# Performance work log

Measured on AMD Instinct MI355X. Metric: run time of the kernel, lower is better.

The kernel has to match this reference:

```python
import jax, jax.numpy as jnp
import numpy as np

EMB_SIZE = 768
BLOCK_SIZE = 64
OFFSET = 1  # bert cls offset


def setup_inputs() -> dict:
    key = jax.random.key(0)
    ks = jax.random.split(key, 10)
    n, c, d, h, E, M, P = 4, 1024, 768, 12, 42, 8, 1024
    sequence_output = jax.random.normal(ks[0], (n, c, d), jnp.float32)
    attention = jax.random.uniform(ks[1], (n, h, c, c), jnp.float32)
    attention = attention / attention.sum(-1, keepdims=True)  # softmax-like rows
    Wh = jax.random.normal(ks[2], (EMB_SIZE, 2 * d), jnp.float32) * 0.02
    bh = jax.random.normal(ks[3], (EMB_SIZE,), jnp.float32) * 0.02
    Wt = jax.random.normal(ks[4], (EMB_SIZE, 2 * d), jnp.float32) * 0.02
    bt = jax.random.normal(ks[5], (EMB_SIZE,), jnp.float32) * 0.02
    Wb = jax.random.normal(ks[6], (99, EMB_SIZE * BLOCK_SIZE), jnp.float32) * 0.02
    mention_pos = jax.random.randint(ks[7], (n, E, M), 0, c - 1 - OFFSET, jnp.int32)
    mention_mask = jax.random.randint(ks[8], (n, E, M), 0, 2, jnp.int32)
    mention_mask = mention_mask.at[:, :, 0].set(1)  # every entity has >=1 mention
    hts = jax.random.randint(ks[9], (n, P, 2), 0, E, jnp.int32)
    return {"sequence_output": sequence_output, "attention": attention,
            "Wh": Wh, "bh": bh, "Wt": Wt, "bt": bt, "Wb": Wb,
            "mention_pos": mention_pos, "mention_mask": mention_mask, "hts": hts}


def _get_hrt_doc(seq, att, pos, mask, ht):
    # seq [c,d], att [h,c,c], pos/mask [E,M], ht [P,2]
    p = pos + OFFSET                                   # [E,M]
    valid = mask > 0
    memb = seq[p]                                      # [E,M,d] gather
    e_emb = jax.scipy.special.logsumexp(
        jnp.where(valid[..., None], memb, -jnp.inf), axis=1)  # [E,d]
    matt = att[:, p]                                   # [h,E,M,c] gather
    cnt = valid.sum(1).astype(seq.dtype)               # [E]
    e_att = (matt * valid[None, :, :, None].astype(seq.dtype)).sum(2)
    e_att = jnp.transpose(e_att, (1, 0, 2)) / cnt[:, None, None]  # [E,h,c] mention mean
    hs = e_emb[ht[:, 0]]                               # [P,d]
    ts = e_emb[ht[:, 1]]
    h_att = e_att[ht[:, 0]]                            # [P,h,c]
    t_att = e_att[ht[:, 1]]
    ht_att = (h_att * t_att).mean(1)                   # [P,c] head mean
    ht_att = ht_att / (ht_att.sum(1, keepdims=True) + 1e-5)
    rs = jnp.einsum('ld,rl->rd', seq, ht_att)          # [P,d]
    return hs, ts, rs


def reference(sequence_output, attention, Wh, bh, Wt, bt, Wb,
              mention_pos, mention_mask, hts):
    d = sequence_output.shape[-1]
    hs, ts, rs = jax.vmap(_get_hrt_doc)(sequence_output, attention,
                                        mention_pos, mention_mask, hts)
    hs = hs.reshape(-1, d)
    ts = ts.reshape(-1, d)
    rs = rs.reshape(-1, d)
    hs = jnp.tanh(jnp.concatenate([hs, rs], axis=1) @ Wh.T + bh)
    ts = jnp.tanh(jnp.concatenate([ts, rs], axis=1) @ Wt.T + bt)
    nb = EMB_SIZE // BLOCK_SIZE
    b1 = hs.reshape(-1, nb, BLOCK_SIZE)
    b2 = ts.reshape(-1, nb, BLOCK_SIZE)
    bl = (b1[:, :, :, None] * b2[:, :, None, :]).reshape(-1, EMB_SIZE * BLOCK_SIZE)
    logits = bl @ Wb.T                                 # [N, num_labels+2]
    return logits
```

## Files before the change

kernel.cpp:

```cpp
#include <hip/hip_runtime.h>
#include <hip/hip_bf16.h>
#include <hip/hip_fp16.h>
#include <math.h>

#define NDOC 4
#define CCC  1024
#define DDD  768
#define HHH  12
#define EEE  42
#define MMM  8
#define PPP  1024
#define NK   99
#define NPAD 112
#define NSLICE 24

typedef __attribute__((ext_vector_type(8))) short short8v;
typedef __attribute__((ext_vector_type(8))) _Float16 half8;
typedef __attribute__((ext_vector_type(4))) float floatx4;

__device__ __forceinline__ unsigned short f32_to_bf16u(float f) {
  return __builtin_bit_cast(unsigned short, __float2bfloat16(f));
}
__device__ __forceinline__ unsigned short f32_to_f16u(float f) {
  return __builtin_bit_cast(unsigned short, __float2half(f));
}

__global__ __launch_bounds__(256) void k_prep(
    const float* __restrict__ seq, const float* __restrict__ att,
    const float* __restrict__ Wh, const float* __restrict__ Wt,
    const float* __restrict__ Wb,
    const int* __restrict__ pos, const int* __restrict__ mask,
    unsigned short* __restrict__ eembB, float* __restrict__ eatt,
    unsigned short* __restrict__ WhtB, unsigned short* __restrict__ seqTB,
    unsigned short* __restrict__ WpB) {
  const int bx = blockIdx.x;
  const int tid = threadIdx.x;
  if (bx < 168) {
    int e = bx % EEE, doc = bx / EEE;
    int base = (doc*EEE + e)*MMM;
    int p[MMM], mk[MMM];
#pragma unroll
    for (int m = 0; m < MMM; ++m) { p[m] = pos[base+m] + 1; mk[m] = mask[base+m]; }
    for (int d0 = tid; d0 < DDD; d0 += 256) {
      float v[MMM]; float mx = -INFINITY;
#pragma unroll
      for (int m = 0; m < MMM; ++m) {
        v[m] = seq[(doc*CCC + p[m])*DDD + d0];
        if (mk[m]) mx = fmaxf(mx, v[m]);
      }
      float s = 0.f;
#pragma unroll
      for (int m = 0; m < MMM; ++m) if (mk[m]) s += expf(v[m]-mx);
      eembB[(doc*EEE + e)*DDD + d0] = f32_to_bf16u(logf(s) + mx);
    }
  } else if (bx < 2184) {
    int b = bx - 168;
    int head = b % HHH, e = (b/HHH) % EEE, doc = b / (HHH*EEE);
    int base = (doc*EEE + e)*MMM;
    int j = tid * 4;
    float ax=0.f, ay=0.f, az=0.f, aw=0.f; float cnt = 0.f;
#pragma unroll
    for (int m = 0; m < MMM; ++m) {
      int mk = mask[base+m];
      cnt += (float)mk;
      if (mk) {
        int pp = pos[base+m] + 1;
        const float4 a = *(const float4*)&att[((size_t)(doc*HHH + head)*CCC + pp)*CCC + j];
        ax += a.x; ay += a.y; az += a.z; aw += a.w;
      }
    }
    float inv = 1.f / cnt;
    float4 o; o.x = ax*inv; o.y = ay*inv; o.z = az*inv; o.w = aw*inv;
    *(float4*)&eatt[((size_t)((doc*EEE + e)*HHH + head))*CCC + j] = o;
  } else if (bx < 3336) {
    int gid = (bx - 2184)*256 + tid;
    int half = gid >= 147456;
    int loc = half ? gid - 147456 : gid;
    const float* src = (half ? Wt : Wh) + (size_t)loc*8;
    float4 v0 = *(const float4*)src;
    float4 v1 = *(const float4*)(src+4);
    unsigned short o[8];
    o[0]=f32_to_bf16u(v0.x); o[1]=f32_to_bf16u(v0.y); o[2]=f32_to_bf16u(v0.z); o[3]=f32_to_bf16u(v0.w);
    o[4]=f32_to_bf16u(v1.x); o[5]=f32_to_bf16u(v1.y); o[6]=f32_to_bf16u(v1.z); o[7]=f32_to_bf16u(v1.w);
    *(uint4*)&WhtB[(size_t)half*1179648 + (size_t)loc*8] = *(const uint4*)o;
  } else if (bx < 4104) {
    __shared__ float tl[64][65];
    int b = bx - 3336;
    int d0 = (b % 12)*64, c0 = ((b/12) % 16)*64, doc = b / 192;
#pragma unroll
    for (int rep = 0; rep < 4; ++rep) {
      int cr = rep*16 + (tid >> 4);
      int d4 = (tid & 15) * 4;
      float4 v = *(const float4*)&seq[((size_t)doc*CCC + c0 + cr)*DDD + d0 + d4];
      tl[cr][d4+0]=v.x; tl[cr][d4+1]=v.y; tl[cr][d4+2]=v.z; tl[cr][d4+3]=v.w;
    }
    __syncthreads();
#pragma unroll
    for (int rep = 0; rep < 4; ++rep) {
      int dr = rep*16 + (tid >> 4);
      int c4 = (tid & 15) * 4;
      unsigned short o[4];
#pragma unroll
      for (int kq = 0; kq < 4; ++kq)
        o[kq] = f32_to_bf16u(tl[c4+kq][dr]);
      *(uint2*)&seqTB[((size_t)doc*DDD + d0 + dr)*CCC + c0 + c4] = *(const uint2*)o;
    }
  } else {
    int t = (bx - 4104)*256 + tid;
    int j8 = (t & 7) * 8;
    int n = (t >> 3) % NPAD;
    int ki = t / 896;
    unsigned short o[8];
    if (n < NK) {
      const float* src = &Wb[(size_t)n*49152 + ki*64 + j8];
      float4 v0 = *(const float4*)src;
      float4 v1 = *(const float4*)(src+4);
      o[0]=f32_to_f16u(v0.x); o[1]=f32_to_f16u(v0.y); o[2]=f32_to_f16u(v0.z); o[3]=f32_to_f16u(v0.w);
      o[4]=f32_to_f16u(v1.x); o[5]=f32_to_f16u(v1.y); o[6]=f32_to_f16u(v1.z); o[7]=f32_to_f16u(v1.w);
    } else {
#pragma unroll
      for (int e=0;e<8;++e) o[e]=0;
    }
    int js = (t & 7) >> 2, q = t & 3;
    int nt = n >> 4, lnn = n & 15;
    int c = ((js*7 + nt)*4 + q)*16 + lnn;
    *(uint4*)&WpB[(size_t)ki*7168 + c*8] = *(const uint4*)o;
  }
}

__global__ __launch_bounds__(256) void k_htatt1(const float* __restrict__ eatt,
    const int* __restrict__ hts, float* __restrict__ htU,
    float* __restrict__ Ssum) {
  __shared__ float tile[EEE*16*12];
  const int cg = blockIdx.x, doc = blockIdx.y;
  const int c0 = cg * 16;
  for (int idx = threadIdx.x; idx < EEE*16*12; idx += 256) {
    int e = idx / 192, rem = idx % 192, h = rem / 16, cc = rem % 16;
    tile[(e*16 + cc)*12 + h] =
        eatt[((size_t)((doc*EEE + e)*HHH + h))*CCC + c0 + cc];
  }
  __syncthreads();
  const int cc = threadIdx.x & 15;
  const int pg = threadIdx.x >> 4;
  for (int it = 0; it < 64; ++it) {
    int p = pg + it*16;
    int h0 = hts[(doc*PPP + p)*2 + 0];
    int t0 = hts[(doc*PPP + p)*2 + 1];
    const float* a = &tile[(h0*16 + cc)*12];
    const float* b = &tile[(t0*16 + cc)*12];
    float4 a0 = *(const float4*)a,     b0 = *(const float4*)b;
    float4 a1 = *(const float4*)(a+4), b1 = *(const float4*)(b+4);
    float4 a2 = *(const float4*)(a+8), b2 = *(const float4*)(b+8);
    float s = a0.x*b0.x + a0.y*b0.y + a0.z*b0.z + a0.w*b0.w
            + a1.x*b1.x + a1.y*b1.y + a1.z*b1.z + a1.w*b1.w
            + a2.x*b2.x + a2.y*b2.y + a2.z*b2.z + a2.w*b2.w;
    s *= (1.f/12.f);
    htU[((size_t)(doc*PPP + p))*CCC + c0 + cc] = s;
    float r = s;
    r += __shfl_xor(r, 1, 16);
    r += __shfl_xor(r, 2, 16);
    r += __shfl_xor(r, 4, 16);
    r += __shfl_xor(r, 8, 16);
    if (cc == 0) Ssum[((size_t)(doc*PPP + p))*64 + cg] = r;
  }
}

__global__ __launch_bounds__(256) void k_htnorm(const float* __restrict__ htU,
    const float* __restrict__ Ssum, unsigned short* __restrict__ htB) {
  __shared__ float sc_sh;
  const int b = blockIdx.x;
  const int lane = threadIdx.x;
  if (lane < 64) {
    float r = Ssum[(size_t)b*64 + lane];
    for (int off = 32; off > 0; off >>= 1) r += __shfl_down(r, off, 64);
    if (lane == 0) sc_sh = 1.f / (r + 1e-5f);
  }
  __syncthreads();
  float sc = sc_sh;
  float4 v = *(const float4*)&htU[(size_t)b*CCC + lane*4];
  unsigned short o[4];
  o[0] = f32_to_bf16u(v.x*sc); o[1] = f32_to_bf16u(v.y*sc);
  o[2] = f32_to_bf16u(v.z*sc); o[3] = f32_to_bf16u(v.w*sc);
  *(uint2*)&htB[(size_t)b*CCC + lane*4] = *(const uint2*)o;
}

__global__ __launch_bounds__(256) void k_rs_mfma(
    const unsigned short* __restrict__ htB,
    const unsigned short* __restrict__ seqTB,
    unsigned short* __restrict__ rsB) {
  __shared__ unsigned short A_l[4096];
  __shared__ unsigned short B_l[4096];
  const int n0 = blockIdx.x * 128;
  const int m0 = blockIdx.y * 128;
  const int doc = m0 >> 10;
  const int mloc = m0 & 1023;
  const int t = threadIdx.x;
  const int lane = t & 63;
  const int ln = lane & 15, q4 = lane >> 4;
  const int w = t >> 6;
  const int wr = w >> 1, wc = w & 1;

  const int r0 = t >> 2;
  const int koff = (t & 3) * 8;
  const unsigned short* srcA0 = htB + ((size_t)doc*CCC + mloc + r0)*CCC + koff;
  const unsigned short* srcA1 = htB + ((size_t)doc*CCC + mloc + r0 + 64)*CCC + koff;
  const unsigned short* srcB0 = seqTB + ((size_t)doc*DDD + n0 + r0)*CCC + koff;
  const unsigned short* srcB1 = seqTB + ((size_t)doc*DDD + n0 + r0 + 64)*CCC + koff;

  floatx4 acc[4][4];
#pragma unroll
  for (int i = 0; i < 4; ++i)
#pragma unroll
    for (int j = 0; j < 4; ++j) acc[i][j] = (floatx4){0.f,0.f,0.f,0.f};

  for (int k0 = 0; k0 < CCC; k0 += 32) {
    uint4 va0 = *(const uint4*)(srcA0 + k0);
    uint4 va1 = *(const uint4*)(srcA1 + k0);
    uint4 vb0 = *(const uint4*)(srcB0 + k0);
    uint4 vb1 = *(const uint4*)(srcB1 + k0);
    __syncthreads();
    *(uint4*)&A_l[(size_t)t*8]       = va0;
    *(uint4*)&A_l[(size_t)(t+256)*8] = va1;
    *(uint4*)&B_l[(size_t)t*8]       = vb0;
    *(uint4*)&B_l[(size_t)(t+256)*8] = vb1;
    __syncthreads();
    short8v a[4], b[4];
#pragma unroll
    for (int rt = 0; rt < 4; ++rt)
      a[rt] = *(const short8v*)&A_l[((wr*64 + rt*16 + ln)*4 + q4)*8];
#pragma unroll
    for (int nt = 0; nt < 4; ++nt)
      b[nt] = *(const short8v*)&B_l[((wc*64 + nt*16 + ln)*4 + q4)*8];
#pragma unroll
    for (int rt = 0; rt < 4; ++rt)
#pragma unroll
      for (int nt = 0; nt < 4; ++nt)
        acc[rt][nt] = __builtin_amdgcn_mfma_f32_16x16x32_bf16(a[rt], b[nt], acc[rt][nt], 0, 0, 0);
  }
#pragma unroll
  for (int rt = 0; rt < 4; ++rt)
#pragma unroll
    for (int nt = 0; nt < 4; ++nt) {
      int col = n0 + wc*64 + nt*16 + ln;
#pragma unroll
      for (int reg = 0; reg < 4; ++reg) {
        int row = m0 + wr*64 + rt*16 + q4*4 + reg;
        rsB[(size_t)row*DDD + col] = f32_to_bf16u(acc[rt][nt][reg]);
      }
    }
}

__global__ __launch_bounds__(256) void k_heads_mfma(
    const unsigned short* __restrict__ eembB,
    const unsigned short* __restrict__ rsB,
    const int* __restrict__ hts,
    const unsigned short* __restrict__ WB,
    const float* __restrict__ bh, const float* __restrict__ bt,
    unsigned short* __restrict__ hsTB,
    unsigned short* __restrict__ tsbH) {
  __shared__ unsigned short A_l[4096];
  __shared__ unsigned short B_l[4096];
  __shared__ unsigned short T_l[128*144];
  const int which = blockIdx.z;
  const int n0 = blockIdx.x * 128;
  const int m0 = blockIdx.y * 128;
  const int doc = m0 >> 10;
  const int t = threadIdx.x;
  const int lane = t & 63;
  const int ln = lane & 15, q4 = lane >> 4;
  const int w = t >> 6;
  const int wr = w >> 1, wc = w & 1;

  const int r0 = t >> 2;
  const int koff = (t & 3) * 8;
  const int rgA0 = m0 + r0, rgA1 = m0 + r0 + 64;
  const int idx0 = hts[rgA0*2 + which];
  const int idx1 = hts[rgA1*2 + which];
  const unsigned short* srcE0 = eembB + (size_t)(doc*EEE + idx0)*DDD + koff;
  const unsigned short* srcE1 = eembB + (size_t)(doc*EEE + idx1)*DDD + koff;
  const unsigned short* srcR0 = rsB + (size_t)rgA0*DDD + koff;
  const unsigned short* srcR1 = rsB + (size_t)rgA1*DDD + koff;
  const unsigned short* WBz = WB + (size_t)which*1179648;
  const unsigned short* srcW0 = WBz + (size_t)(n0 + r0)*1536 + koff;
  const unsigned short* srcW1 = WBz + (size_t)(n0 + r0 + 64)*1536 + koff;

  floatx4 acc[4][4];
#pragma unroll
  for (int i = 0; i < 4; ++i)
#pragma unroll
    for (int j = 0; j < 4; ++j) acc[i][j] = (floatx4){0.f,0.f,0.f,0.f};

  for (int k0 = 0; k0 < 1536; k0 += 32) {
    uint4 va0 = (k0 < DDD) ? *(const uint4*)(srcE0 + k0) : *(const uint4*)(srcR0 + (k0 - DDD));
    uint4 va1 = (k0 < DDD) ? *(const uint4*)(srcE1 + k0) : *(const uint4*)(srcR1 + (k0 - DDD));
    uint4 vb0 = *(const uint4*)(srcW0 + k0);
    uint4 vb1 = *(const uint4*)(srcW1 + k0);
    __syncthreads();
    *(uint4*)&A_l[(size_t)t*8]       = va0;
    *(uint4*)&A_l[(size_t)(t+256)*8] = va1;
    *(uint4*)&B_l[(size_t)t*8]       = vb0;
    *(uint4*)&B_l[(size_t)(t+256)*8] = vb1;
    __syncthreads();
    short8v a[4], b[4];
#pragma unroll
    for (int rt = 0; rt < 4; ++rt)
      a[rt] = *(const short8v*)&A_l[((wr*64 + rt*16 + ln)*4 + q4)*8];
#pragma unroll
    for (int nt = 0; nt < 4; ++nt)
      b[nt] = *(const short8v*)&B_l[((wc*64 + nt*16 + ln)*4 + q4)*8];
#pragma unroll
    for (int rt = 0; rt < 4; ++rt)
#pragma unroll
      for (int nt = 0; nt < 4; ++nt)
        acc[rt][nt] = __builtin_amdgcn_mfma_f32_16x16x32_bf16(a[rt], b[nt], acc[rt][nt], 0, 0, 0);
  }
  const float* bias = which ? bt : bh;
  if (which == 0) {
#pragma unroll
    for (int rt = 0; rt < 4; ++rt)
#pragma unroll
      for (int nt = 0; nt < 4; ++nt) {
        int col = wc*64 + nt*16 + ln;
        float bsv = bias[n0 + col];
#pragma unroll
        for (int reg = 0; reg < 4; ++reg) {
          int row = wr*64 + rt*16 + q4*4 + reg;
          T_l[col*144 + row] = f32_to_f16u(tanhf(acc[rt][nt][reg] + bsv));
        }
      }
    __syncthreads();
#pragma unroll
    for (int iter = 0; iter < 8; ++iter) {
      int col = iter*16 + (t >> 4);
      int rblk = t & 15;
      uint4 v = *(const uint4*)&T_l[col*144 + rblk*8];
      *(uint4*)&hsTB[(size_t)(n0 + col)*4096 + m0 + rblk*8] = v;
    }
  } else {
#pragma unroll
    for (int rt = 0; rt < 4; ++rt)
#pragma unroll
      for (int nt = 0; nt < 4; ++nt) {
        int col = n0 + wc*64 + nt*16 + ln;
        float bsv = bias[col];
#pragma unroll
        for (int reg = 0; reg < 4; ++reg) {
          int row = m0 + wr*64 + rt*16 + q4*4 + reg;
          tsbH[(size_t)row*DDD + col] = f32_to_f16u(tanhf(acc[rt][nt][reg] + bsv));
        }
      }
  }
}

__global__ __launch_bounds__(128) void k_logits_mfma(
    const unsigned short* __restrict__ hsT,
    const unsigned short* __restrict__ tsbH,
    const unsigned short* __restrict__ Wp,
    unsigned short* __restrict__ P) {
  __shared__ unsigned short hsT_l[32*128];
  __shared__ unsigned short Bt_l[2*7168];
  const int slice = blockIdx.x;
  const int kbase = (slice >> 1)*64 + (slice & 1)*32;
  const int nb = slice >> 1;
  const int mtile = blockIdx.y;
  const int t = threadIdx.x;
  const int w = t >> 6;
  const int lane = t & 63;
  const int ln = lane & 15;
  const int q = lane >> 4;
  const int m0w = mtile*128 + w*64;

#pragma unroll
  for (int rep = 0; rep < 4; ++rep) {
    int c16 = t + rep*128;
    int ii = c16 >> 4;
    int c8 = (c16 & 15) * 8;
    uint4 v = *(const uint4*)&hsT[(size_t)(kbase + ii)*4096 + mtile*128 + c8];
    *(uint4*)&hsT_l[ii*128 + c8] = v;
  }

  __half2 tsr2[4][2][4];
#pragma unroll
  for (int rt = 0; rt < 4; ++rt) {
    int row = m0w + rt*16 + ln;
#pragma unroll
    for (int js = 0; js < 2; ++js) {
      uint4 v = *(const uint4*)&tsbH[(size_t)row*DDD + nb*64 + js*32 + q*8];
      tsr2[rt][js][0] = __builtin_bit_cast(__half2, v.x);
      tsr2[rt][js][1] = __builtin_bit_cast(__half2, v.y);
      tsr2[rt][js][2] = __builtin_bit_cast(__half2, v.z);
      tsr2[rt][js][3] = __builtin_bit_cast(__half2, v.w);
    }
  }

  floatx4 acc[4][7];
#pragma unroll
  for (int rt = 0; rt < 4; ++rt)
#pragma unroll
    for (int nt = 0; nt < 7; ++nt)
      acc[rt][nt] = (floatx4){0.f,0.f,0.f,0.f};

  uint4 wreg[7];
#pragma unroll
  for (int r = 0; r < 7; ++r)
    wreg[r] = *(const uint4*)&Wp[(size_t)kbase*7168 + (t + r*128)*8];
#pragma unroll
  for (int r = 0; r < 7; ++r)
    *(uint4*)&Bt_l[(t + r*128)*8] = wreg[r];
  __syncthreads();

  for (int ii = 0; ii < 32; ++ii) {
    const unsigned short* bufc = Bt_l + (ii & 1)*7168;
    if (ii < 31) {
      int ki = kbase + ii + 1;
#pragma unroll
      for (int r = 0; r < 7; ++r)
        wreg[r] = *(const uint4*)&Wp[(size_t)ki*7168 + (t + r*128)*8];
    }
    __half2 hh[4];
#pragma unroll
    for (int rt = 0; rt < 4; ++rt) {
      unsigned short hb = hsT_l[ii*128 + w*64 + rt*16 + ln];
      hh[rt] = __half2half2(__ushort_as_half(hb));
    }
#pragma unroll
    for (int js = 0; js < 2; ++js) {
      half8 a[4];
#pragma unroll
      for (int rt = 0; rt < 4; ++rt) {
        uint4 au;
        au.x = __builtin_bit_cast(unsigned int, __hmul2(hh[rt], tsr2[rt][js][0]));
        au.y = __builtin_bit_cast(unsigned int, __hmul2(hh[rt], tsr2[rt][js][1]));
        au.z = __builtin_bit_cast(unsigned int, __hmul2(hh[rt], tsr2[rt][js][2]));
        au.w = __builtin_bit_cast(unsigned int, __hmul2(hh[rt], tsr2[rt][js][3]));
        a[rt] = __builtin_bit_cast(half8, au);
      }
#pragma unroll
      for (int nt = 0; nt < 7; ++nt) {
        half8 b = __builtin_bit_cast(half8,
            *(const short8v*)&bufc[((js*7 + nt)*4)*128 + lane*8]);
#pragma unroll
        for (int rt = 0; rt < 4; ++rt)
          acc[rt][nt] = __builtin_amdgcn_mfma_f32_16x16x32_f16(a[rt], b, acc[rt][nt], 0, 0, 0);
      }
    }
    if (ii < 31) {
      __syncthreads();
#pragma unroll
      for (int r = 0; r < 7; ++r)
        *(uint4*)&Bt_l[((ii+1) & 1)*7168 + (t + r*128)*8] = wreg[r];
      __syncthreads();
    }
  }

  unsigned short* Ps = P + (size_t)slice*(4096*NPAD);
#pragma unroll
  for (int nt = 0; nt < 7; ++nt) {
    int col = nt*16 + ln;
#pragma unroll
    for (int rt = 0; rt < 4; ++rt) {
#pragma unroll
      for (int reg = 0; reg < 4; ++reg) {
        int row = m0w + rt*16 + q*4 + reg;
        Ps[(size_t)row*NPAD + col] = f32_to_f16u(acc[rt][nt][reg]);
      }
    }
  }
}

__global__ __launch_bounds__(256) void k_logred(const unsigned short* __restrict__ P,
    float* __restrict__ out) {
  int idx = blockIdx.x*256 + threadIdx.x;
  int r = idx / NPAD;
  int c = idx % NPAD;
  if (c >= NK) return;
  float s = 0.f;
#pragma unroll
  for (int sl = 0; sl < NSLICE; ++sl)
    s += __half2float(__ushort_as_half(P[(size_t)sl*(4096*NPAD) + idx]));
  out[(size_t)r*NK + c] = s;
}

extern "C" void kernel_launch(void* const* d_in, const int* in_sizes, int n_in,
                              void* d_out, int out_size, void* d_ws, size_t ws_size,
                              hipStream_t stream) {
  const float* seq  = (const float*)d_in[0];
  const float* att  = (const float*)d_in[1];
  const float* Wh   = (const float*)d_in[2];
  const float* bh   = (const float*)d_in[3];
  const float* Wt   = (const float*)d_in[4];
  const float* bt   = (const float*)d_in[5];
  const float* Wb   = (const float*)d_in[6];
  const int* pos    = (const int*)d_in[7];
  const int* mask   = (const int*)d_in[8];
  const int* hts    = (const int*)d_in[9];
  float* out = (float*)d_out;

  float* ws = (float*)d_ws;
  float*          eatt  = ws;
  float*          htU   = ws + 2064384;
  float*          Ssum  = ws + 6258688;
  unsigned short* htB   = (unsigned short*)(ws + 6520832);
  unsigned short* eembB = (unsigned short*)(ws + 8617984);
  unsigned short* seqTB = (unsigned short*)(ws + 8682496);
  unsigned short* WhtB  = (unsigned short*)(ws + 10255360);
  unsigned short* rsB   = (unsigned short*)(ws + 11435008);
  unsigned short* hsTB  = (unsigned short*)(ws + 13007872);
  unsigned short* tsbH  = (unsigned short*)(ws + 14580736);
  unsigned short* WpB   = (unsigned short*)(ws + 16153600);
  unsigned short* Pp    = (unsigned short*)(ws + 18906112);

  k_prep<<<dim3(6792), 256, 0, stream>>>(seq, att, Wh, Wt, Wb, pos, mask,
                                         eembB, eatt, WhtB, seqTB, WpB);
  k_htatt1<<<dim3(64, NDOC), 256, 0, stream>>>(eatt, hts, htU, Ssum);
  k_htnorm<<<dim3(NDOC*PPP), 256, 0, stream>>>(htU, Ssum, htB);
  k_rs_mfma<<<dim3(6, 32), 256, 0, stream>>>(htB, seqTB, rsB);
  k_heads_mfma<<<dim3(6, 32, 2), 256, 0, stream>>>(eembB, rsB, hts, WhtB, bh, bt, hsTB, tsbH);
  k_logits_mfma<<<dim3(NSLICE, 32), 128, 0, stream>>>(hsTB, tsbH, WpB, Pp);
  k_logred<<<dim3(4096*NPAD/256), 256, 0, stream>>>(Pp, out);
}
```

Measured before the change: 264.7 us.

## Split logits K into 96 slices and read Wb fragments directly from global

The logits GEMM now splits K into 96 slices of 8 instead of 24 slices of 32, so the grid has four times as many blocks. The LDS double buffer and the barrier-synchronised refill of Wb are removed, and each wave loads its B fragments straight from global memory into registers. The Wb repack kernel's thread mapping is reordered to read Wb more contiguously. In exchange, the split-K partial buffer and the final reduction grow fourfold, adding global write and read traffic.

```diff
diff --git a/kernel.cpp b/kernel.cpp
--- a/kernel.cpp
+++ b/kernel.cpp
@@ -12,7 +12,7 @@
 #define PPP  1024
 #define NK   99
 #define NPAD 112
-#define NSLICE 24
+#define NSLICE 96
 
 typedef __attribute__((ext_vector_type(8))) short short8v;
 typedef __attribute__((ext_vector_type(8))) _Float16 half8;
@@ -107,9 +107,10 @@
     }
   } else {
     int t = (bx - 4104)*256 + tid;
-    int j8 = (t & 7) * 8;
-    int n = (t >> 3) % NPAD;
-    int ki = t / 896;
+    int n  = t / 6144;
+    int rem = t % 6144;
+    int ki = rem >> 3;
+    int j8 = (rem & 7) * 8;
     unsigned short o[8];
     if (n < NK) {
       const float* src = &Wb[(size_t)n*49152 + ki*64 + j8];
@@ -121,7 +122,7 @@
 #pragma unroll
       for (int e=0;e<8;++e) o[e]=0;
     }
-    int js = (t & 7) >> 2, q = t & 3;
+    int js = j8 >> 5, q = (j8 >> 3) & 3;
     int nt = n >> 4, lnn = n & 15;
     int c = ((js*7 + nt)*4 + q)*16 + lnn;
     *(uint4*)&WpB[(size_t)ki*7168 + c*8] = *(const uint4*)o;
@@ -357,11 +358,10 @@
     const unsigned short* __restrict__ tsbH,
     const unsigned short* __restrict__ Wp,
     unsigned short* __restrict__ P) {
-  __shared__ unsigned short hsT_l[32*128];
-  __shared__ unsigned short Bt_l[2*7168];
+  __shared__ unsigned short hsT_l[8*128];
   const int slice = blockIdx.x;
-  const int kbase = (slice >> 1)*64 + (slice & 1)*32;
-  const int nb = slice >> 1;
+  const int kbase = slice * 8;
+  const int nb = slice >> 3;
   const int mtile = blockIdx.y;
   const int t = threadIdx.x;
   const int w = t >> 6;
@@ -370,11 +370,9 @@
   const int q = lane >> 4;
   const int m0w = mtile*128 + w*64;
 
-#pragma unroll
-  for (int rep = 0; rep < 4; ++rep) {
-    int c16 = t + rep*128;
-    int ii = c16 >> 4;
-    int c8 = (c16 & 15) * 8;
+  {
+    int ii = t >> 4;
+    int c8 = (t & 15) * 8;
     uint4 v = *(const uint4*)&hsT[(size_t)(kbase + ii)*4096 + mtile*128 + c8];
     *(uint4*)&hsT_l[ii*128 + c8] = v;
   }
@@ -400,23 +398,11 @@
     for (int nt = 0; nt < 7; ++nt)
       acc[rt][nt] = (floatx4){0.f,0.f,0.f,0.f};
 
-  uint4 wreg[7];
-#pragma unroll
-  for (int r = 0; r < 7; ++r)
-    wreg[r] = *(const uint4*)&Wp[(size_t)kbase*7168 + (t + r*128)*8];
-#pragma unroll
-  for (int r = 0; r < 7; ++r)
-    *(uint4*)&Bt_l[(t + r*128)*8] = wreg[r];
   __syncthreads();
 
-  for (int ii = 0; ii < 32; ++ii) {
-    const unsigned short* bufc = Bt_l + (ii & 1)*7168;
-    if (ii < 31) {
-      int ki = kbase + ii + 1;
-#pragma unroll
-      for (int r = 0; r < 7; ++r)
-        wreg[r] = *(const uint4*)&Wp[(size_t)ki*7168 + (t + r*128)*8];
-    }
+  const unsigned short* wb = Wp + (size_t)kbase*7168;
+#pragma unroll
+  for (int ii = 0; ii < 8; ++ii) {
     __half2 hh[4];
 #pragma unroll
     for (int rt = 0; rt < 4; ++rt) {
@@ -425,6 +411,11 @@
     }
 #pragma unroll
     for (int js = 0; js < 2; ++js) {
+      half8 b[7];
+#pragma unroll
+      for (int nt = 0; nt < 7; ++nt)
+        b[nt] = __builtin_bit_cast(half8,
+            *(const uint4*)&wb[((size_t)ii*896 + (js*7 + nt)*64 + lane)*8]);
       half8 a[4];
 #pragma unroll
       for (int rt = 0; rt < 4; ++rt) {
@@ -436,20 +427,10 @@
         a[rt] = __builtin_bit_cast(half8, au);
       }
 #pragma unroll
-      for (int nt = 0; nt < 7; ++nt) {
-        half8 b = __builtin_bit_cast(half8,
-            *(const short8v*)&bufc[((js*7 + nt)*4)*128 + lane*8]);
+      for (int nt = 0; nt < 7; ++nt)
 #pragma unroll
         for (int rt = 0; rt < 4; ++rt)
-          acc[rt][nt] = __builtin_amdgcn_mfma_f32_16x16x32_f16(a[rt], b, acc[rt][nt], 0, 0, 0);
-      }
-    }
-    if (ii < 31) {
-      __syncthreads();
-#pragma unroll
-      for (int r = 0; r < 7; ++r)
-        *(uint4*)&Bt_l[((ii+1) & 1)*7168 + (t + r*128)*8] = wreg[r];
-      __syncthreads();
+          acc[rt][nt] = __builtin_amdgcn_mfma_f32_16x16x32_f16(a[rt], b[nt], acc[rt][nt], 0, 0, 0);
     }
   }
 
@@ -475,7 +456,7 @@
   int c = idx % NPAD;
   if (c >= NK) return;
   float s = 0.f;
-#pragma unroll
+#pragma unroll 8
   for (int sl = 0; sl < NSLICE; ++sl)
     s += __half2float(__ushort_as_half(P[(size_t)sl*(4096*NPAD) + idx]));
   out[(size_t)r*NK + c] = s;
```

New measurement: 257.8 us. -2.6%, faster.
